# Performance work log

Measured on AMD Instinct MI355X. Metric: run time of the kernel, lower is better.

Reference implementation:

```python
import jax, jax.numpy as jnp
import numpy as np

DIM = 256
NUM_HEADS = 8
HEAD_DIM = DIM // NUM_HEADS
CPB_HIDDEN = 512
B, N = 2, 2304
TABLE = 9025  # (2*48-1)**2


def _l2norm(t, eps=1e-12):
    # matches torch F.normalize(dim=-1): x / max(||x||, eps)
    n = jnp.sqrt(jnp.sum(t * t, axis=-1, keepdims=True))
    return t / jnp.maximum(n, eps)


def setup_inputs() -> dict:
    key = jax.random.key(0)
    ks = jax.random.split(key, 12)
    x = jax.random.normal(ks[0], (B, N, DIM), dtype=jnp.float32)
    relative_pos_index = jax.random.randint(ks[1], (N, N), 0, TABLE, dtype=jnp.int64)
    relative_coords_table = jax.random.uniform(ks[2], (TABLE, 2), dtype=jnp.float32) * 2.0 - 1.0
    seq_length_scale = jnp.ones((1,), dtype=jnp.float32) * jnp.log2(jnp.float32(N))
    padding_mask = jnp.zeros((B, N), dtype=jnp.int32)
    s = 0.02
    W_qkv = jax.random.normal(ks[3], (3 * DIM, DIM), dtype=jnp.float32) * s
    b_qkv = jnp.zeros((3 * DIM,), dtype=jnp.float32)
    # temperature init: log(exp(1/0.24) - 1) so softplus(temperature) = 1/0.24
    temperature = jnp.full((NUM_HEADS, 1, 1), float(np.log(np.expm1(1.0 / 0.24))), dtype=jnp.float32)
    query_embedding = jax.random.normal(ks[4], (NUM_HEADS, 1, HEAD_DIM), dtype=jnp.float32) * s
    W_proj = jax.random.normal(ks[5], (DIM, DIM), dtype=jnp.float32) * s
    b_proj = jnp.zeros((DIM,), dtype=jnp.float32)
    W_cpb1 = jax.random.normal(ks[6], (CPB_HIDDEN, 2), dtype=jnp.float32) * s
    b_cpb1 = jnp.zeros((CPB_HIDDEN,), dtype=jnp.float32)
    W_cpb2 = jax.random.normal(ks[7], (NUM_HEADS, CPB_HIDDEN), dtype=jnp.float32) * s
    b_cpb2 = jnp.zeros((NUM_HEADS,), dtype=jnp.float32)
    return {
        'x': x, 'relative_pos_index': relative_pos_index,
        'relative_coords_table': relative_coords_table,
        'seq_length_scale': seq_length_scale, 'padding_mask': padding_mask,
        'W_qkv': W_qkv, 'b_qkv': b_qkv, 'temperature': temperature,
        'query_embedding': query_embedding, 'W_proj': W_proj, 'b_proj': b_proj,
        'W_cpb1': W_cpb1, 'b_cpb1': b_cpb1, 'W_cpb2': W_cpb2, 'b_cpb2': b_cpb2,
    }


def reference(x, relative_pos_index, relative_coords_table, seq_length_scale,
              padding_mask, W_qkv, b_qkv, temperature, query_embedding,
              W_proj, b_proj, W_cpb1, b_cpb1, W_cpb2, b_cpb2):
    Bx, Nx, C = x.shape
    h, d = NUM_HEADS, HEAD_DIM
    # qkv projection -> (B, 3h, N, d); first h heads = q, then k, then v
    qkv = (jnp.einsum('bnc,oc->bno', x, W_qkv) + b_qkv)
    qkv = qkv.reshape(Bx, Nx, 3 * h, d).transpose(0, 2, 1, 3)
    q, k, v = qkv[:, :h], qkv[:, h:2 * h], qkv[:, 2 * h:]
    # CPB relative bias: (T,2) -> (T,h) -> (h,N,N) via gather
    hid = jax.nn.relu(relative_coords_table @ W_cpb1.T + b_cpb1)
    tab = hid @ W_cpb2.T + b_cpb2                    # (T, h)
    rel_bias = tab.T[:, relative_pos_index.reshape(-1)].reshape(h, Nx, Nx)
    # cosine-sim attention with learned query embedding + softplus temperature
    scale = jax.nn.softplus(temperature) * seq_length_scale[0]   # (h,1,1)
    qn = (_l2norm(q) + query_embedding) * scale                  # (B,h,N,d)
    kn = _l2norm(k)
    attn = jnp.einsum('bhnd,bhmd->bhnm', qn, kn) + rel_bias
    attn = jax.nn.softmax(attn, axis=-1)
    out = jnp.einsum('bhnm,bhmd->bhnd', attn, v)
    out = out.transpose(0, 2, 1, 3).reshape(Bx, Nx, C)
    out = out @ W_proj.T + b_proj
    return out
```

## Files before the change

### kernel.cpp

```cpp
#include <hip/hip_runtime.h>
#include <math.h>

#define DIMC 256
#define NHEADS 8
#define HDIM 32
#define CPBH 512
#define BB 2
#define NSEQ 2304
#define TAB 9025
#define TABP 9040
#define RTOT (BB*NHEADS*NSEQ)
#define SPLITS 4
#define MSP (NSEQ/SPLITS)
#define PBS 36
#define NCHUNK (NSEQ/32)
#define LOG2E 1.44269504088896340736f

#define NWQ (3*DIMC*DIMC)
#define IDXP_ELEMS    (NSEQ * NCHUNK * 16)
#define IDXP4_BLOCKS  (IDXP_ELEMS / 1024)
#define CPB_BLOCKS    ((TAB + 63) / 64)
#define QKV_BLOCKS    (12 * 72)

typedef unsigned short ushort;
typedef __attribute__((ext_vector_type(8))) short short8;
typedef __attribute__((ext_vector_type(4))) short short4v;
typedef __attribute__((ext_vector_type(4))) float f32x4;

#define MFMA16(a,b,c) __builtin_amdgcn_mfma_f32_16x16x32_bf16((a),(b),(c),0,0,0)

__device__ __forceinline__ ushort f2bf(float x) {
  unsigned u = __float_as_uint(x);
  u += 0x7FFFu + ((u >> 16) & 1u);
  return (ushort)(u >> 16);
}
__device__ __forceinline__ float bf2f(ushort b) {
  return __uint_as_float(((unsigned)b) << 16);
}
__device__ __forceinline__ float fexp2(float x) {
#if defined(__has_builtin)
#if __has_builtin(__builtin_amdgcn_exp2f)
  return __builtin_amdgcn_exp2f(x);
#else
  return exp2f(x);
#endif
#else
  return exp2f(x);
#endif
}
__device__ __forceinline__ unsigned pack_trunc(float p0, float p1) {
  return __builtin_amdgcn_perm(__float_as_uint(p1), __float_as_uint(p0), 0x07060302u);
}
__device__ __forceinline__ void cvt8(const float* __restrict__ p, short8* hi, short8* lo) {
  float4 v0 = *(const float4*)p;
  float4 v1 = *(const float4*)(p + 4);
  float vv[8] = {v0.x, v0.y, v0.z, v0.w, v1.x, v1.y, v1.z, v1.w};
  short8 h, l;
#pragma unroll
  for (int i = 0; i < 8; ++i) {
    ushort hh = f2bf(vv[i]);
    h[i] = (short)hh;
    l[i] = (short)f2bf(vv[i] - bf2f(hh));
  }
  *hi = h; *lo = l;
}

__launch_bounds__(256)
__global__ void pre_kernel(const float* __restrict__ x, const float* __restrict__ wq,
                           const int* __restrict__ idx,
                           const float* __restrict__ tbl, const float* __restrict__ W1,
                           const float* __restrict__ b1, const float* __restrict__ W2,
                           const float* __restrict__ b2,
                           const float* __restrict__ bias, const float* __restrict__ temp,
                           const float* __restrict__ sls, const float* __restrict__ qe,
                           ushort* __restrict__ qhi, ushort* __restrict__ qlo,
                           ushort* __restrict__ khi, ushort* __restrict__ klo,
                           ushort* __restrict__ vT,
                           unsigned* __restrict__ idxP, ushort* __restrict__ tabBf) {
  __shared__ __align__(16) float smem[8192];
  int blk = blockIdx.x;
  int tid = threadIdx.x;

  if (blk < CPB_BLOCKS) {
    float* w1b = smem;
    float* w2t = smem + 2048;
    float* part = smem + 6144;
    for (int i = tid; i < CPBH; i += 256) {
      w1b[i * 4 + 0] = W1[2 * i];
      w1b[i * 4 + 1] = W1[2 * i + 1];
      w1b[i * 4 + 2] = b1[i];
      w1b[i * 4 + 3] = 0.f;
    }
    for (int i = tid; i < CPBH * NHEADS; i += 256)
      w2t[(i & (CPBH - 1)) * NHEADS + (i >> 9)] = W2[i];
    int tl = tid & 63, jc = tid >> 6;
    int t = blk * 64 + tl;
    bool valid = t < TAB;
    float c0 = 0.f, c1 = 0.f;
    if (valid) { c0 = tbl[2 * t]; c1 = tbl[2 * t + 1]; }
    __syncthreads();
    float acc[NHEADS];
#pragma unroll
    for (int h = 0; h < NHEADS; ++h) acc[h] = 0.f;
    for (int j = jc * 128; j < jc * 128 + 128; ++j) {
      float4 wv = *(const float4*)&w1b[j * 4];
      float hid = fmaxf(fmaf(c0, wv.x, fmaf(c1, wv.y, wv.z)), 0.f);
      float4 wa = *(const float4*)&w2t[j * NHEADS];
      float4 wb = *(const float4*)&w2t[j * NHEADS + 4];
      acc[0] = fmaf(hid, wa.x, acc[0]);
      acc[1] = fmaf(hid, wa.y, acc[1]);
      acc[2] = fmaf(hid, wa.z, acc[2]);
      acc[3] = fmaf(hid, wa.w, acc[3]);
      acc[4] = fmaf(hid, wb.x, acc[4]);
      acc[5] = fmaf(hid, wb.y, acc[5]);
      acc[6] = fmaf(hid, wb.z, acc[6]);
      acc[7] = fmaf(hid, wb.w, acc[7]);
    }
#pragma unroll
    for (int h = 0; h < NHEADS; ++h) part[((size_t)jc * 64 + tl) * NHEADS + h] = acc[h];
    __syncthreads();
    if (jc == 0 && valid) {
#pragma unroll
      for (int h = 0; h < NHEADS; ++h) {
        float s = b2[h];
#pragma unroll
        for (int p = 0; p < 4; ++p) s += part[((size_t)p * 64 + tl) * NHEADS + h];
        tabBf[h * TABP + t] = f2bf(s * LOG2E);
      }
    }
  } else if (blk < CPB_BLOCKS + QKV_BLOCKS) {
    float (*vbuf)[65] = (float(*)[65])smem;
    int t = blk - CPB_BLOCKS;
    int n0 = (t % 12) * 64, m0 = (t / 12) * 64;
    int lane = tid & 63, w = tid >> 6;
    int g = lane >> 4, c = lane & 15;
    int mw = m0 + w * 16;
    const int K = DIMC;
    f32x4 acc[4] = {{0,0,0,0},{0,0,0,0},{0,0,0,0},{0,0,0,0}};
#pragma unroll 2
    for (int k0 = 0; k0 < K; k0 += 32) {
      short8 ah, al;
      cvt8(&x[(size_t)(mw + c) * K + k0 + g * 8], &ah, &al);
#pragma unroll
      for (int nt = 0; nt < 4; ++nt) {
        short8 bh, bl;
        cvt8(&wq[(size_t)(n0 + nt * 16 + c) * K + k0 + g * 8], &bh, &bl);
        acc[nt] = MFMA16(ah, bh, acc[nt]);
        acc[nt] = MFMA16(al, bh, acc[nt]);
        acc[nt] = MFMA16(ah, bl, acc[nt]);
      }
    }
#pragma unroll
    for (int nt = 0; nt < 4; ++nt) {
      float bv = bias[n0 + nt * 16 + c];
#pragma unroll
      for (int r = 0; r < 4; ++r) acc[nt][r] += bv;
    }

    int b = (m0 >= NSEQ) ? 1 : 0;
    int nb = m0 - b * NSEQ;
    int sect = n0 >> 8;
    int hloc = (n0 & 255) >> 5;

    if (sect < 2) {
#pragma unroll
      for (int H = 0; H < 2; ++H) {
        int head = hloc + H;
        float scale = (sect == 0) ? log1pf(expf(temp[head])) * sls[0] * LOG2E : 0.f;
#pragma unroll
        for (int r = 0; r < 4; ++r) {
          float ss = acc[2*H][r]*acc[2*H][r] + acc[2*H+1][r]*acc[2*H+1][r];
          ss += __shfl_xor(ss, 1);
          ss += __shfl_xor(ss, 2);
          ss += __shfl_xor(ss, 4);
          ss += __shfl_xor(ss, 8);
          float inv = 1.f / fmaxf(sqrtf(ss), 1e-12f);
#pragma unroll
          for (int half = 0; half < 2; ++half) {
            int d = half * 16 + c;
            float val = acc[2*H + half][r] * inv;
            if (sect == 0) val = (val + qe[head * HDIM + d]) * scale;
            vbuf[w * 16 + g * 4 + r][H * 32 + d] = val;
          }
        }
      }
      __syncthreads();
      int plane = tid >> 7;
      int seg = tid & 127;
      int head = seg >> 6, row = seg & 63;
      const float* srcrow = &vbuf[row][head * 32];
      ushort out16[32];
#pragma unroll
      for (int i = 0; i < 32; ++i) {
        float v = srcrow[i];
        ushort hh = f2bf(v);
        out16[i] = plane ? f2bf(v - bf2f(hh)) : hh;
      }
      ushort* dstp = plane ? (sect == 0 ? qlo : klo) : (sect == 0 ? qhi : khi);
      size_t off = ((size_t)(b * NHEADS + hloc + head) * NSEQ + nb + row) * HDIM;
#pragma unroll
      for (int q4 = 0; q4 < 4; ++q4)
        *(int4*)&dstp[off + q4 * 8] = ((int4*)out16)[q4];
    } else {
#pragma unroll
      for (int nt = 0; nt < 4; ++nt)
#pragma unroll
        for (int r = 0; r < 4; ++r)
          vbuf[w * 16 + g * 4 + r][nt * 16 + c] = acc[nt][r];
      __syncthreads();
      int hbase = (n0 - 512) >> 5;
#pragma unroll
      for (int it = 0; it < 16; ++it) {
        int dloc = (tid >> 6) * 16 + it;
        int p = tid & 63;
        int pp = p & 31;
        int nsrc = (p & 32) + (pp & 1) * 16 + (pp >> 1);
        float v = vbuf[nsrc][dloc];
        int head = hbase + (dloc >> 5), d = dloc & 31;
        vT[((size_t)((b * NHEADS + head) * HDIM + d)) * NSEQ + nb + p] = f2bf(v);
      }
    }
  } else {
    int t4 = (blk - CPB_BLOCKS - QKV_BLOCKS) * 256 + tid;
    int grp = t4 >> 4;
    int ch = grp % NCHUNK;
    int n4 = grp / NCHUNK;
    int m = ch * 32 + (t4 & 15);
    unsigned o[4];
#pragma unroll
    for (int i = 0; i < 4; ++i) {
      unsigned lo = (unsigned)idx[(size_t)(n4 * 4 + i) * NSEQ + m];
      unsigned hi = (unsigned)idx[(size_t)(n4 * 4 + i) * NSEQ + m + 16];
      o[i] = lo | (hi << 16);
    }
    *(uint4*)&idxP[(size_t)t4 * 4] = *(const uint4*)o;
  }
}

__launch_bounds__(256)
__global__ void attn_kernel(const ushort* __restrict__ qhi, const ushort* __restrict__ qlo,
                            const ushort* __restrict__ khi, const ushort* __restrict__ klo,
                            const ushort* __restrict__ vT, const ushort* __restrict__ tabBf,
                            const unsigned* __restrict__ idxP,
                            float* __restrict__ pO, float* __restrict__ pL) {
  __shared__ ushort tbf[10240];
  __shared__ __align__(16) ushort pbuf[8][16 * PBS];
  int tid = threadIdx.x;
  int lane = tid & 63;
  int w = tid >> 6;
  int qb = blockIdx.x;
  int by = blockIdx.y;
  int s = by & 3, bh = by >> 2;
  int h = bh & (NHEADS - 1);

  const ushort* tsrc = tabBf + h * TABP;
#pragma unroll
  for (int i = 0; i < 5; ++i) {
    int off = i * 2048 + tid * 8;
    *(int4*)&tbf[off] = *(const int4*)&tsrc[off];
  }

  int g = lane >> 4, c = lane & 15;
  int q0 = qb * 128 + w * 16;
  int q1 = q0 + 64;
  int qg0 = q0 >> 2, qg1 = q1 >> 2;
  size_t rowbase = (size_t)bh * NSEQ;

  short8 qAh = *(const short8*)&qhi[(rowbase + q0 + c) * HDIM + g * 8];
  short8 qAl = *(const short8*)&qlo[(rowbase + q0 + c) * HDIM + g * 8];
  short8 qBh = *(const short8*)&qhi[(rowbase + q1 + c) * HDIM + g * 8];
  short8 qBl = *(const short8*)&qlo[(rowbase + q1 + c) * HDIM + g * 8];
  __syncthreads();

  short one = (c == 0) ? (short)0x3F80 : (short)0;
  short8 onesB = {one, one, one, one, one, one, one, one};

  f32x4 oa0 = {0,0,0,0}, oa1 = {0,0,0,0}, ob0 = {0,0,0,0}, ob1 = {0,0,0,0};
  f32x4 la = {0,0,0,0}, lb = {0,0,0,0};
  ushort* pba = pbuf[w * 2];
  ushort* pbb = pbuf[w * 2 + 1];
  int m0 = s * MSP;

#define LOADK(MT, D0H, D0L, D1H, D1L, IA, IB) do {                    \
    size_t ra_ = (rowbase + (MT) + c) * HDIM + g * 8;                 \
    D0H = *(const short8*)&khi[ra_];                                  \
    D0L = *(const short8*)&klo[ra_];                                  \
    D1H = *(const short8*)&khi[ra_ + 16 * HDIM];                      \
    D1L = *(const short8*)&klo[ra_ + 16 * HDIM];                      \
    size_t ia_ = ((size_t)(qg0 + g) * NCHUNK + ((MT) >> 5)) * 64 + c * 4; \
    IA = *(const uint4*)&idxP[ia_];                                   \
    size_t ib_ = ((size_t)(qg1 + g) * NCHUNK + ((MT) >> 5)) * 64 + c * 4; \
    IB = *(const uint4*)&idxP[ib_];                                   \
  } while (0)
#define LOADV(MT, V0, V1) do {                                        \
    size_t va_ = ((size_t)(bh * HDIM + c)) * NSEQ + (MT) + g * 8;     \
    V0 = *(const short8*)&vT[va_];                                    \
    V1 = *(const short8*)&vT[va_ + 16 * NSEQ];                        \
  } while (0)

  short8 c0h, c0l, c1h, c1l, vf0, vf1;
  uint4 ia, ib;
  LOADK(m0, c0h, c0l, c1h, c1l, ia, ib);
  LOADV(m0, vf0, vf1);

  for (int mt = m0; mt < m0 + MSP; mt += 32) {
    int mtn = (mt + 32 < m0 + MSP) ? (mt + 32) : m0;
    short8 n0h, n0l, n1h, n1l, u0, u1;
    uint4 ja, jb;
    LOADK(mtn, n0h, n0l, n1h, n1l, ja, jb);
    LOADV(mtn, u0, u1);

    f32x4 sa0 = {0,0,0,0}, sa1 = {0,0,0,0}, sb0 = {0,0,0,0}, sb1 = {0,0,0,0};
    __builtin_amdgcn_s_setprio(1);
    sa0 = MFMA16(qAh, c0h, sa0);
    sb0 = MFMA16(qBh, c0h, sb0);
    sa1 = MFMA16(qAh, c1h, sa1);
    sb1 = MFMA16(qBh, c1h, sb1);
    sa0 = MFMA16(qAl, c0h, sa0);
    sb0 = MFMA16(qBl, c0h, sb0);
    sa1 = MFMA16(qAl, c1h, sa1);
    sb1 = MFMA16(qBl, c1h, sb1);
    sa0 = MFMA16(qAh, c0l, sa0);
    sb0 = MFMA16(qBh, c0l, sb0);
    sa1 = MFMA16(qAh, c1l, sa1);
    sb1 = MFMA16(qBh, c1l, sb1);
    __builtin_amdgcn_s_setprio(0);

    unsigned ipa[4] = {ia.x, ia.y, ia.z, ia.w};
    unsigned ipb[4] = {ib.x, ib.y, ib.z, ib.w};
#pragma unroll
    for (int r = 0; r < 4; ++r) {
      int k0 = ipa[r] & 0xFFFF, k1 = ipa[r] >> 16;
      float pA0 = fexp2(sa0[r] + bf2f(tbf[k0]));
      float pA1 = fexp2(sa1[r] + bf2f(tbf[k1]));
      *(unsigned*)&pba[(g * 4 + r) * PBS + 2 * c] = pack_trunc(pA0, pA1);
    }
#pragma unroll
    for (int r = 0; r < 4; ++r) {
      int k0 = ipb[r] & 0xFFFF, k1 = ipb[r] >> 16;
      float pB0 = fexp2(sb0[r] + bf2f(tbf[k0]));
      float pB1 = fexp2(sb1[r] + bf2f(tbf[k1]));
      *(unsigned*)&pbb[(g * 4 + r) * PBS + 2 * c] = pack_trunc(pB0, pB1);
    }

    short4v paA = *(const short4v*)&pba[c * PBS + g * 8];
    short4v paB = *(const short4v*)&pba[c * PBS + g * 8 + 4];
    short8 pfa = __builtin_shufflevector(paA, paB, 0, 1, 2, 3, 4, 5, 6, 7);
    short4v pbA = *(const short4v*)&pbb[c * PBS + g * 8];
    short4v pbB = *(const short4v*)&pbb[c * PBS + g * 8 + 4];
    short8 pfb = __builtin_shufflevector(pbA, pbB, 0, 1, 2, 3, 4, 5, 6, 7);

    __builtin_amdgcn_s_setprio(1);
    oa0 = MFMA16(pfa, vf0, oa0);
    oa1 = MFMA16(pfa, vf1, oa1);
    ob0 = MFMA16(pfb, vf0, ob0);
    ob1 = MFMA16(pfb, vf1, ob1);
    la  = MFMA16(pfa, onesB, la);
    lb  = MFMA16(pfb, onesB, lb);
    __builtin_amdgcn_s_setprio(0);

    c0h = n0h; c0l = n0l; c1h = n1h; c1l = n1l;
    vf0 = u0; vf1 = u1;
    ia = ja; ib = jb;
  }
#undef LOADK
#undef LOADV

  size_t prow0 = (size_t)s * RTOT + rowbase;
#pragma unroll
  for (int r = 0; r < 4; ++r) {
    size_t pra = prow0 + q0 + g * 4 + r;
    pO[pra * HDIM + c]      = oa0[r];
    pO[pra * HDIM + 16 + c] = oa1[r];
    size_t prb = prow0 + q1 + g * 4 + r;
    pO[prb * HDIM + c]      = ob0[r];
    pO[prb * HDIM + 16 + c] = ob1[r];
    if (c == 0) { pL[pra] = la[r]; pL[prb] = lb[r]; }
  }
}

#define ALD 264
__launch_bounds__(256)
__global__ void gemm_proj_fused(const float* __restrict__ pO, const float* __restrict__ pL,
                                const float* __restrict__ Wp,
                                const float* __restrict__ bias, float* __restrict__ C) {
  __shared__ __align__(16) ushort Ahs[64 * ALD];
  __shared__ __align__(16) ushort Als[64 * ALD];
  int tid = threadIdx.x;
  int m0 = blockIdx.x * 64;
  int b = (m0 >= NSEQ) ? 1 : 0;
  int nb = m0 - b * NSEQ;

  {
    int r = tid >> 2;
    int q = tid & 3;
    int n = nb + r;
#pragma unroll
    for (int h = 0; h < NHEADS; ++h) {
      size_t bhn = (size_t)(b * NHEADS + h) * NSEQ + n;
      float L = 0.f;
#pragma unroll
      for (int sp = 0; sp < SPLITS; ++sp) L += pL[(size_t)sp * RTOT + bhn];
      float inv = 1.f / L;
      float a[8] = {0.f, 0.f, 0.f, 0.f, 0.f, 0.f, 0.f, 0.f};
#pragma unroll
      for (int sp = 0; sp < SPLITS; ++sp) {
        const float* src = &pO[((size_t)sp * RTOT + bhn) * HDIM + q * 8];
        float4 v0 = *(const float4*)&src[0];
        float4 v1 = *(const float4*)&src[4];
        a[0] += v0.x; a[1] += v0.y; a[2] += v0.z; a[3] += v0.w;
        a[4] += v1.x; a[5] += v1.y; a[6] += v1.z; a[7] += v1.w;
      }
      ushort hi8[8], lo8[8];
#pragma unroll
      for (int i = 0; i < 8; ++i) {
        float v = a[i] * inv;
        ushort hh = f2bf(v);
        hi8[i] = hh;
        lo8[i] = f2bf(v - bf2f(hh));
      }
      int k = h * 32 + q * 8;
      *(int4*)&Ahs[r * ALD + k] = *(int4*)hi8;
      *(int4*)&Als[r * ALD + k] = *(int4*)lo8;
    }
  }
  __syncthreads();

  int lane = tid & 63, w = tid >> 6;
  int g = lane >> 4, c = lane & 15;
  int n0 = w * 64;
  f32x4 acc[4][4] = {};
  for (int k0 = 0; k0 < DIMC; k0 += 32) {
    short8 bfh[4], bfl[4];
#pragma unroll
    for (int nt = 0; nt < 4; ++nt)
      cvt8(&Wp[(size_t)(n0 + nt * 16 + c) * DIMC + k0 + g * 8], &bfh[nt], &bfl[nt]);
#pragma unroll
    for (int mt = 0; mt < 4; ++mt) {
      short8 ah = *(const short8*)&Ahs[(mt * 16 + c) * ALD + k0 + g * 8];
      short8 al = *(const short8*)&Als[(mt * 16 + c) * ALD + k0 + g * 8];
#pragma unroll
      for (int nt = 0; nt < 4; ++nt) {
        acc[mt][nt] = MFMA16(ah, bfh[nt], acc[mt][nt]);
        acc[mt][nt] = MFMA16(al, bfh[nt], acc[mt][nt]);
        acc[mt][nt] = MFMA16(ah, bfl[nt], acc[mt][nt]);
      }
    }
  }
#pragma unroll
  for (int nt = 0; nt < 4; ++nt) {
    float bv = bias[n0 + nt * 16 + c];
#pragma unroll
    for (int mt = 0; mt < 4; ++mt)
#pragma unroll
      for (int r = 0; r < 4; ++r)
        C[(size_t)(m0 + mt * 16 + g * 4 + r) * DIMC + n0 + nt * 16 + c] = acc[mt][nt][r] + bv;
  }
}

extern "C" void kernel_launch(void* const* d_in, const int* in_sizes, int n_in,
                              void* d_out, int out_size, void* d_ws, size_t ws_size,
                              hipStream_t stream) {
  const float* x    = (const float*)d_in[0];
  const int*   idx  = (const int*)d_in[1];
  const float* tbl  = (const float*)d_in[2];
  const float* sls  = (const float*)d_in[3];
  const float* Wqkv = (const float*)d_in[5];
  const float* bqkv = (const float*)d_in[6];
  const float* temp = (const float*)d_in[7];
  const float* qe   = (const float*)d_in[8];
  const float* Wp   = (const float*)d_in[9];
  const float* bp   = (const float*)d_in[10];
  const float* W1   = (const float*)d_in[11];
  const float* b1   = (const float*)d_in[12];
  const float* W2   = (const float*)d_in[13];
  const float* b2   = (const float*)d_in[14];

  float* ws   = (float*)d_ws;
  float* pO   = ws;
  float* pL   = pO + (size_t)SPLITS * RTOT * HDIM;
  unsigned* idxP = (unsigned*)(pL + (size_t)SPLITS * RTOT);
  ushort* u   = (ushort*)(idxP + IDXP_ELEMS);
  ushort* qhi = u;                u += (size_t)RTOT * HDIM;
  ushort* qlo = u;                u += (size_t)RTOT * HDIM;
  ushort* khi = u;                u += (size_t)RTOT * HDIM;
  ushort* klo = u;                u += (size_t)RTOT * HDIM;
  ushort* vT  = u;                u += (size_t)RTOT * HDIM;
  ushort* tabBf = u;              u += 73728;
  float* out  = (float*)d_out;

  pre_kernel<<<dim3(CPB_BLOCKS + QKV_BLOCKS + IDXP4_BLOCKS), dim3(256), 0, stream>>>(
      x, Wqkv, idx, tbl, W1, b1, W2, b2, bqkv, temp, sls, qe,
      qhi, qlo, khi, klo, vT, idxP, tabBf);
  attn_kernel<<<dim3(NSEQ / 128, BB * NHEADS * SPLITS), dim3(256), 0, stream>>>(
      qhi, qlo, khi, klo, vT, tabBf, idxP, pO, pL);
  gemm_proj_fused<<<dim3((BB * NSEQ) / 64), dim3(256), 0, stream>>>(
      pO, pL, Wp, bp, out);
}
```

Baseline: 214.5 us.

## Pair both batches per block to share bias gathers and remap attention grid

The attention kernel now gives each block both batch elements of the same head and query rows. The relative-bias index loads and LDS table lookups are then done once and reused for both batches, instead of loading separate index data for two query groups of one batch. The grid becomes one-dimensional with a swizzled head/split mapping. The kernel drops the software-prefetched K/V registers in favour of direct per-iteration loads and adds an occupancy hint (launch_bounds 256,4). The projection GEMM uses 32-row tiles to double the block count, which reduces per-block LDS but re-reads the weights more often.

Result: slower. 270.1 us (+26.0%).

```diff
diff --git a/kernel.cpp b/kernel.cpp
--- a/kernel.cpp
+++ b/kernel.cpp
@@ -237,7 +237,7 @@
   }
 }
 
-__launch_bounds__(256)
+__launch_bounds__(256, 4)
 __global__ void attn_kernel(const ushort* __restrict__ qhi, const ushort* __restrict__ qlo,
                             const ushort* __restrict__ khi, const ushort* __restrict__ klo,
                             const ushort* __restrict__ vT, const ushort* __restrict__ tabBf,
@@ -248,10 +248,13 @@
   int tid = threadIdx.x;
   int lane = tid & 63;
   int w = tid >> 6;
-  int qb = blockIdx.x;
-  int by = blockIdx.y;
-  int s = by & 3, bh = by >> 2;
-  int h = bh & (NHEADS - 1);
+
+  int bid = blockIdx.x;
+  int qb = bid >> 5;
+  int k8 = bid & 7;
+  int j4 = (bid >> 3) & 3;
+  int y  = k8 + 8 * j4;
+  int s = y & 3, h = y >> 2;
 
   const ushort* tsrc = tabBf + h * TABP;
 #pragma unroll
@@ -261,15 +264,15 @@
   }
 
   int g = lane >> 4, c = lane & 15;
-  int q0 = qb * 128 + w * 16;
-  int q1 = q0 + 64;
-  int qg0 = q0 >> 2, qg1 = q1 >> 2;
-  size_t rowbase = (size_t)bh * NSEQ;
-
-  short8 qAh = *(const short8*)&qhi[(rowbase + q0 + c) * HDIM + g * 8];
-  short8 qAl = *(const short8*)&qlo[(rowbase + q0 + c) * HDIM + g * 8];
-  short8 qBh = *(const short8*)&qhi[(rowbase + q1 + c) * HDIM + g * 8];
-  short8 qBl = *(const short8*)&qlo[(rowbase + q1 + c) * HDIM + g * 8];
+  int q0 = qb * 64 + w * 16;
+  int qg0 = q0 >> 2;
+  size_t rowA = (size_t)h * NSEQ;
+  size_t rowB = (size_t)(NHEADS + h) * NSEQ;
+
+  short8 qAh = *(const short8*)&qhi[(rowA + q0 + c) * HDIM + g * 8];
+  short8 qAl = *(const short8*)&qlo[(rowA + q0 + c) * HDIM + g * 8];
+  short8 qBh = *(const short8*)&qhi[(rowB + q0 + c) * HDIM + g * 8];
+  short8 qBl = *(const short8*)&qlo[(rowB + q0 + c) * HDIM + g * 8];
   __syncthreads();
 
   short one = (c == 0) ? (short)0x3F80 : (short)0;
@@ -281,65 +284,65 @@
   ushort* pbb = pbuf[w * 2 + 1];
   int m0 = s * MSP;
 
-#define LOADK(MT, D0H, D0L, D1H, D1L, IA, IB) do {                    \
-    size_t ra_ = (rowbase + (MT) + c) * HDIM + g * 8;                 \
-    D0H = *(const short8*)&khi[ra_];                                  \
-    D0L = *(const short8*)&klo[ra_];                                  \
-    D1H = *(const short8*)&khi[ra_ + 16 * HDIM];                      \
-    D1L = *(const short8*)&klo[ra_ + 16 * HDIM];                      \
-    size_t ia_ = ((size_t)(qg0 + g) * NCHUNK + ((MT) >> 5)) * 64 + c * 4; \
-    IA = *(const uint4*)&idxP[ia_];                                   \
-    size_t ib_ = ((size_t)(qg1 + g) * NCHUNK + ((MT) >> 5)) * 64 + c * 4; \
-    IB = *(const uint4*)&idxP[ib_];                                   \
-  } while (0)
-#define LOADV(MT, V0, V1) do {                                        \
-    size_t va_ = ((size_t)(bh * HDIM + c)) * NSEQ + (MT) + g * 8;     \
-    V0 = *(const short8*)&vT[va_];                                    \
-    V1 = *(const short8*)&vT[va_ + 16 * NSEQ];                        \
-  } while (0)
-
-  short8 c0h, c0l, c1h, c1l, vf0, vf1;
-  uint4 ia, ib;
-  LOADK(m0, c0h, c0l, c1h, c1l, ia, ib);
-  LOADV(m0, vf0, vf1);
+  unsigned oKA = (unsigned)((rowA + m0 + c) * HDIM + g * 8);
+  unsigned oKB = (unsigned)((rowB + m0 + c) * HDIM + g * 8);
+  unsigned oVA = (unsigned)(((unsigned)(h * HDIM + c)) * NSEQ + m0 + g * 8);
+  unsigned oVB = (unsigned)(((unsigned)((NHEADS + h) * HDIM + c)) * NSEQ + m0 + g * 8);
+  unsigned oIb = (unsigned)(((unsigned)(qg0 + g) * NCHUNK + (m0 >> 5)) * 64 + c * 4);
+  unsigned oI  = oIb;
+
+  uint4 ia = *(const uint4*)&idxP[oI];
 
   for (int mt = m0; mt < m0 + MSP; mt += 32) {
-    int mtn = (mt + 32 < m0 + MSP) ? (mt + 32) : m0;
-    short8 n0h, n0l, n1h, n1l, u0, u1;
-    uint4 ja, jb;
-    LOADK(mtn, n0h, n0l, n1h, n1l, ja, jb);
-    LOADV(mtn, u0, u1);
+    unsigned oIn = (mt + 32 < m0 + MSP) ? oI + 64 : oIb;
+    uint4 ian = *(const uint4*)&idxP[oIn];
+    oI = oIn;
+
+    unsigned ip[4] = {ia.x, ia.y, ia.z, ia.w};
+    float b0[4], b1[4];
+#pragma unroll
+    for (int r = 0; r < 4; ++r) {
+      b0[r] = bf2f(tbf[ip[r] & 0xFFFF]);
+      b1[r] = bf2f(tbf[ip[r] >> 16]);
+    }
+
+    short8 ak0h = *(const short8*)&khi[oKA];
+    short8 ak0l = *(const short8*)&klo[oKA];
+    short8 ak1h = *(const short8*)&khi[oKA + 16 * HDIM];
+    short8 ak1l = *(const short8*)&klo[oKA + 16 * HDIM];
+    short8 bk0h = *(const short8*)&khi[oKB];
+    short8 bk0l = *(const short8*)&klo[oKB];
+    short8 bk1h = *(const short8*)&khi[oKB + 16 * HDIM];
+    short8 bk1l = *(const short8*)&klo[oKB + 16 * HDIM];
+    short8 vf0 = *(const short8*)&vT[oVA];
+    short8 vf1 = *(const short8*)&vT[oVA + 16 * NSEQ];
+    short8 wf0 = *(const short8*)&vT[oVB];
+    short8 wf1 = *(const short8*)&vT[oVB + 16 * NSEQ];
+    oKA += 32 * HDIM; oKB += 32 * HDIM; oVA += 32; oVB += 32;
 
     f32x4 sa0 = {0,0,0,0}, sa1 = {0,0,0,0}, sb0 = {0,0,0,0}, sb1 = {0,0,0,0};
     __builtin_amdgcn_s_setprio(1);
-    sa0 = MFMA16(qAh, c0h, sa0);
-    sb0 = MFMA16(qBh, c0h, sb0);
-    sa1 = MFMA16(qAh, c1h, sa1);
-    sb1 = MFMA16(qBh, c1h, sb1);
-    sa0 = MFMA16(qAl, c0h, sa0);
-    sb0 = MFMA16(qBl, c0h, sb0);
-    sa1 = MFMA16(qAl, c1h, sa1);
-    sb1 = MFMA16(qBl, c1h, sb1);
-    sa0 = MFMA16(qAh, c0l, sa0);
-    sb0 = MFMA16(qBh, c0l, sb0);
-    sa1 = MFMA16(qAh, c1l, sa1);
-    sb1 = MFMA16(qBh, c1l, sb1);
+    sa0 = MFMA16(qAh, ak0h, sa0);
+    sa1 = MFMA16(qAh, ak1h, sa1);
+    sb0 = MFMA16(qBh, bk0h, sb0);
+    sb1 = MFMA16(qBh, bk1h, sb1);
+    sa0 = MFMA16(qAl, ak0h, sa0);
+    sa1 = MFMA16(qAl, ak1h, sa1);
+    sb0 = MFMA16(qBl, bk0h, sb0);
+    sb1 = MFMA16(qBl, bk1h, sb1);
+    sa0 = MFMA16(qAh, ak0l, sa0);
+    sa1 = MFMA16(qAh, ak1l, sa1);
+    sb0 = MFMA16(qBh, bk0l, sb0);
+    sb1 = MFMA16(qBh, bk1l, sb1);
     __builtin_amdgcn_s_setprio(0);
 
-    unsigned ipa[4] = {ia.x, ia.y, ia.z, ia.w};
-    unsigned ipb[4] = {ib.x, ib.y, ib.z, ib.w};
 #pragma unroll
     for (int r = 0; r < 4; ++r) {
-      int k0 = ipa[r] & 0xFFFF, k1 = ipa[r] >> 16;
-      float pA0 = fexp2(sa0[r] + bf2f(tbf[k0]));
-      float pA1 = fexp2(sa1[r] + bf2f(tbf[k1]));
+      float pA0 = fexp2(sa0[r] + b0[r]);
+      float pA1 = fexp2(sa1[r] + b1[r]);
       *(unsigned*)&pba[(g * 4 + r) * PBS + 2 * c] = pack_trunc(pA0, pA1);
-    }
-#pragma unroll
-    for (int r = 0; r < 4; ++r) {
-      int k0 = ipb[r] & 0xFFFF, k1 = ipb[r] >> 16;
-      float pB0 = fexp2(sb0[r] + bf2f(tbf[k0]));
-      float pB1 = fexp2(sb1[r] + bf2f(tbf[k1]));
+      float pB0 = fexp2(sb0[r] + b0[r]);
+      float pB1 = fexp2(sb1[r] + b1[r]);
       *(unsigned*)&pbb[(g * 4 + r) * PBS + 2 * c] = pack_trunc(pB0, pB1);
     }
 
@@ -353,26 +356,23 @@
     __builtin_amdgcn_s_setprio(1);
     oa0 = MFMA16(pfa, vf0, oa0);
     oa1 = MFMA16(pfa, vf1, oa1);
-    ob0 = MFMA16(pfb, vf0, ob0);
-    ob1 = MFMA16(pfb, vf1, ob1);
+    ob0 = MFMA16(pfb, wf0, ob0);
+    ob1 = MFMA16(pfb, wf1, ob1);
     la  = MFMA16(pfa, onesB, la);
     lb  = MFMA16(pfb, onesB, lb);
     __builtin_amdgcn_s_setprio(0);
 
-    c0h = n0h; c0l = n0l; c1h = n1h; c1l = n1l;
-    vf0 = u0; vf1 = u1;
-    ia = ja; ib = jb;
-  }
-#undef LOADK
-#undef LOADV
-
-  size_t prow0 = (size_t)s * RTOT + rowbase;
+    ia = ian;
+  }
+
+  size_t prowA = (size_t)s * RTOT + rowA;
+  size_t prowB = (size_t)s * RTOT + rowB;
 #pragma unroll
   for (int r = 0; r < 4; ++r) {
-    size_t pra = prow0 + q0 + g * 4 + r;
+    size_t pra = prowA + q0 + g * 4 + r;
     pO[pra * HDIM + c]      = oa0[r];
     pO[pra * HDIM + 16 + c] = oa1[r];
-    size_t prb = prow0 + q1 + g * 4 + r;
+    size_t prb = prowB + q0 + g * 4 + r;
     pO[prb * HDIM + c]      = ob0[r];
     pO[prb * HDIM + 16 + c] = ob1[r];
     if (c == 0) { pL[pra] = la[r]; pL[prb] = lb[r]; }
@@ -384,19 +384,21 @@
 __global__ void gemm_proj_fused(const float* __restrict__ pO, const float* __restrict__ pL,
                                 const float* __restrict__ Wp,
                                 const float* __restrict__ bias, float* __restrict__ C) {
-  __shared__ __align__(16) ushort Ahs[64 * ALD];
-  __shared__ __align__(16) ushort Als[64 * ALD];
+  __shared__ __align__(16) ushort Ahs[32 * ALD];
+  __shared__ __align__(16) ushort Als[32 * ALD];
   int tid = threadIdx.x;
-  int m0 = blockIdx.x * 64;
+  int m0 = blockIdx.x * 32;
   int b = (m0 >= NSEQ) ? 1 : 0;
   int nb = m0 - b * NSEQ;
 
   {
-    int r = tid >> 2;
-    int q = tid & 3;
-    int n = nb + r;
-#pragma unroll
-    for (int h = 0; h < NHEADS; ++h) {
+    int rr = tid >> 3;
+    int q  = tid & 3;
+    int hp = (tid >> 2) & 1;
+    int n = nb + rr;
+#pragma unroll
+    for (int hh = 0; hh < 4; ++hh) {
+      int h = hp * 4 + hh;
       size_t bhn = (size_t)(b * NHEADS + h) * NSEQ + n;
       float L = 0.f;
 #pragma unroll
@@ -415,13 +417,13 @@
 #pragma unroll
       for (int i = 0; i < 8; ++i) {
         float v = a[i] * inv;
-        ushort hh = f2bf(v);
-        hi8[i] = hh;
-        lo8[i] = f2bf(v - bf2f(hh));
+        ushort hh2 = f2bf(v);
+        hi8[i] = hh2;
+        lo8[i] = f2bf(v - bf2f(hh2));
       }
       int k = h * 32 + q * 8;
-      *(int4*)&Ahs[r * ALD + k] = *(int4*)hi8;
-      *(int4*)&Als[r * ALD + k] = *(int4*)lo8;
+      *(int4*)&Ahs[rr * ALD + k] = *(int4*)hi8;
+      *(int4*)&Als[rr * ALD + k] = *(int4*)lo8;
     }
   }
   __syncthreads();
@@ -429,14 +431,14 @@
   int lane = tid & 63, w = tid >> 6;
   int g = lane >> 4, c = lane & 15;
   int n0 = w * 64;
-  f32x4 acc[4][4] = {};
+  f32x4 acc[2][4] = {};
   for (int k0 = 0; k0 < DIMC; k0 += 32) {
     short8 bfh[4], bfl[4];
 #pragma unroll
     for (int nt = 0; nt < 4; ++nt)
       cvt8(&Wp[(size_t)(n0 + nt * 16 + c) * DIMC + k0 + g * 8], &bfh[nt], &bfl[nt]);
 #pragma unroll
-    for (int mt = 0; mt < 4; ++mt) {
+    for (int mt = 0; mt < 2; ++mt) {
       short8 ah = *(const short8*)&Ahs[(mt * 16 + c) * ALD + k0 + g * 8];
       short8 al = *(const short8*)&Als[(mt * 16 + c) * ALD + k0 + g * 8];
 #pragma unroll
@@ -451,7 +453,7 @@
   for (int nt = 0; nt < 4; ++nt) {
     float bv = bias[n0 + nt * 16 + c];
 #pragma unroll
-    for (int mt = 0; mt < 4; ++mt)
+    for (int mt = 0; mt < 2; ++mt)
 #pragma unroll
       for (int r = 0; r < 4; ++r)
         C[(size_t)(m0 + mt * 16 + g * 4 + r) * DIMC + n0 + nt * 16 + c] = acc[mt][nt][r] + bv;
@@ -492,8 +494,8 @@
   pre_kernel<<<dim3(CPB_BLOCKS + QKV_BLOCKS + IDXP4_BLOCKS), dim3(256), 0, stream>>>(
       x, Wqkv, idx, tbl, W1, b1, W2, b2, bqkv, temp, sls, qe,
       qhi, qlo, khi, klo, vT, idxP, tabBf);
-  attn_kernel<<<dim3(NSEQ / 128, BB * NHEADS * SPLITS), dim3(256), 0, stream>>>(
+  attn_kernel<<<dim3((NSEQ / 64) * NHEADS * SPLITS), dim3(256), 0, stream>>>(
       qhi, qlo, khi, klo, vT, tabBf, idxP, pO, pL);
-  gemm_proj_fused<<<dim3((BB * NSEQ) / 64), dim3(256), 0, stream>>>(
+  gemm_proj_fused<<<dim3((BB * NSEQ) / 32), dim3(256), 0, stream>>>(
       pO, pL, Wp, bp, out);
 }
```
